# Performance work log

Measured on AMD Instinct MI355X. Metric: run time of the kernel, lower is better.

The kernel has to match this reference:

```python
import jax, jax.numpy as jnp
import numpy as np

HEADS = 16
CHUNK = 128  # chunked (mathematically exact) form of the causal cumsum linear attention
EPS = 0.001


def _linear_attention(q, k, v):
    # q, k, v: (B, H, L, d); q, k already SiLU-featurized
    B, H, L, d = q.shape
    Nc = L // CHUNK
    qc = q.reshape(B, H, Nc, CHUNK, d)
    kc = k.reshape(B, H, Nc, CHUNK, d)
    vc = v.reshape(B, H, Nc, CHUNK, d)

    # inter-chunk running state: S = cumsum of k (x) v over previous chunks, z = cumsum of k
    kv_chunk = jnp.einsum('bhncd,bhnce->bhnde', kc, vc)        # (B,H,Nc,d,d)
    S = jnp.cumsum(kv_chunk, axis=2) - kv_chunk                 # exclusive cumsum
    k_sum = kc.sum(axis=3)                                      # (B,H,Nc,d)
    z = jnp.cumsum(k_sum, axis=2) - k_sum                       # exclusive cumsum

    # intra-chunk causal part
    scores = jnp.einsum('bhnid,bhnjd->bhnij', qc, kc)           # (B,H,Nc,C,C)
    mask = jnp.tril(jnp.ones((CHUNK, CHUNK), dtype=bool))
    scores = jnp.where(mask, scores, jnp.zeros((), scores.dtype))
    num = jnp.einsum('bhnij,bhnje->bhnie', scores, vc)
    num = num + jnp.einsum('bhnid,bhnde->bhnie', qc, S)

    k_cum_local = jnp.cumsum(kc, axis=3)                        # within-chunk cumsum of k
    den = jnp.einsum('bhnid,bhnid->bhni', qc, k_cum_local)
    den = den + jnp.einsum('bhnid,bhnd->bhni', qc, z)

    out = num / jnp.maximum(den, EPS)[..., None]
    return out.reshape(B, H, L, d)


def setup_inputs() -> dict:
    key = jax.random.key(0)
    ks = jax.random.split(key, 9)
    D = 1024
    B, L = 4, 2048
    s = 0.02  # init scale
    return {
        'x':  jax.random.normal(ks[0], (B, L, D), dtype=jnp.float32),
        'Wq': jax.random.normal(ks[1], (D, D), dtype=jnp.float32) * s,
        'bq': jnp.zeros((D,), dtype=jnp.float32),
        'Wk': jax.random.normal(ks[2], (D, D), dtype=jnp.float32) * s,
        'bk': jnp.zeros((D,), dtype=jnp.float32),
        'Wv': jax.random.normal(ks[3], (D, D), dtype=jnp.float32) * s,
        'bv': jnp.zeros((D,), dtype=jnp.float32),
        'Wo': jax.random.normal(ks[4], (D, D), dtype=jnp.float32) * s,
        'bo': jnp.zeros((D,), dtype=jnp.float32),
    }


def reference(x, Wq, bq, Wk, bk, Wv, bv, Wo, bo):
    B, L, D = x.shape
    H = HEADS
    d = D // H
    # torch Linear: y = x @ W.T + b
    q = jax.nn.silu(x @ Wq.T + bq).reshape(B, L, H, d).transpose(0, 2, 1, 3)
    k = jax.nn.silu(x @ Wk.T + bk).reshape(B, L, H, d).transpose(0, 2, 1, 3)
    v = (x @ Wv.T + bv).reshape(B, L, H, d).transpose(0, 2, 1, 3)
    out = _linear_attention(q, k, v)                  # (B,H,L,d)
    out = out.transpose(0, 2, 1, 3).reshape(B, L, D)
    return out @ Wo.T + bo
```

## Files before the change

### kernel.cpp

```cpp
#include <hip/hip_runtime.h>
#include <math.h>

#define D_MODEL 1024
#define HEADS   16
#define HDIM    64
#define CHUNK   128
#define B_SZ    4
#define L_SEQ   2048
#define NCHUNK  16
#define NTOK    8192
#define EPS_DEN 1e-3f

typedef _Float16 half8 __attribute__((ext_vector_type(8)));
typedef float    f32x4 __attribute__((ext_vector_type(4)));

__device__ __forceinline__ void gld_lds16(const void* g, void* l) {
    __builtin_amdgcn_global_load_lds(
        (const __attribute__((address_space(1))) void*)g,
        (__attribute__((address_space(3))) void*)l, 16, 0, 0);
}

__global__ __launch_bounds__(256) void prep(
    const float* __restrict__ x,  const float* __restrict__ Wq,
    const float* __restrict__ Wk, const float* __restrict__ Wv,
    const float* __restrict__ Wo, const float* __restrict__ bq,
    const float* __restrict__ bk,
    _Float16* __restrict__ x2,  _Float16* __restrict__ w2q,
    _Float16* __restrict__ w2k, _Float16* __restrict__ wv16,
    _Float16* __restrict__ wo16, float* __restrict__ bqk) {
    const int bid = blockIdx.x;
    if (bid < 5120) {
        const float* src; _Float16* dst; int t;
        if (bid < 4096)      { src = x;  dst = x2;  t = bid * 256 + threadIdx.x; }
        else if (bid < 4608) { src = Wq; dst = w2q; t = (bid - 4096) * 256 + threadIdx.x; }
        else                 { src = Wk; dst = w2k; t = (bid - 4608) * 256 + threadIdx.x; }
        int m = t >> 7, kc = (t & 127) << 3;
        const float* s = src + (size_t)m * 1024 + kc;
        f32x4 a = *(const f32x4*)s;
        f32x4 b = *(const f32x4*)(s + 4);
        float xs[8] = {a.x, a.y, a.z, a.w, b.x, b.y, b.z, b.w};
        half8 hi, lo;
        #pragma unroll
        for (int u = 0; u < 8; ++u) {
            _Float16 h = (_Float16)xs[u];
            hi[u] = h;
            lo[u] = (_Float16)(xs[u] - (float)h);
        }
        *(half8*)(dst + (size_t)m * 2048 + kc)        = hi;
        *(half8*)(dst + (size_t)m * 2048 + 1024 + kc) = lo;
    } else if (bid < 6144) {
        const float* src; _Float16* dst; int t;
        if (bid < 5632) { src = Wv; dst = wv16; t = (bid - 5120) * 256 + threadIdx.x; }
        else            { src = Wo; dst = wo16; t = (bid - 5632) * 256 + threadIdx.x; }
        int m = t >> 7, kc = (t & 127) << 3;
        const float* s = src + (size_t)m * 1024 + kc;
        f32x4 a = *(const f32x4*)s;
        f32x4 b = *(const f32x4*)(s + 4);
        float xs[8] = {a.x, a.y, a.z, a.w, b.x, b.y, b.z, b.w};
        half8 hv;
        #pragma unroll
        for (int u = 0; u < 8; ++u) hv[u] = (_Float16)xs[u];
        *(half8*)(dst + (size_t)m * 1024 + kc) = hv;
    } else {
        int i = (bid - 6144) * 256 + threadIdx.x;
        bqk[i] = (i < 1024) ? bq[i] : bk[i - 1024];
    }
}

__global__ __launch_bounds__(256, 4) void gemm_qk(
    const _Float16* __restrict__ A,
    const _Float16* __restrict__ B,
    const float* __restrict__ bqk,
    float* __restrict__ Q32, float* __restrict__ K32,
    _Float16* __restrict__ Q16, _Float16* __restrict__ K16) {
    __shared__ __align__(16) _Float16 sA[4096];
    __shared__ __align__(16) _Float16 sB[4096];
    __shared__ __align__(16) _Float16 sC16[32 * 136];

    const int tid  = threadIdx.x;
    const int lane = tid & 63;
    const int w    = tid >> 6;
    const int row0 = blockIdx.x * 128;
    const int col0 = blockIdx.y * 128;
    const int wm   = (w & 1) * 64;
    const int wn   = (w >> 1) * 64;

    const int ch0 = w * 64 + lane;
    const int rS0 = ch0 >> 2;
    const int cS0 = (ch0 & 3) ^ ((rS0 >> 1) & 3);
    const int ch1 = ch0 + 256;
    const int rS1 = ch1 >> 2;
    const int cS1 = (ch1 & 3) ^ ((rS1 >> 1) & 3);

    f32x4 acc[4][4];
    #pragma unroll
    for (int i = 0; i < 4; ++i)
        #pragma unroll
        for (int j = 0; j < 4; ++j) { f32x4 z = {0.f, 0.f, 0.f, 0.f}; acc[i][j] = z; }

    const int ml = lane & 15;
    const int kg = lane >> 4;
    int offA[4], offB[4];
    #pragma unroll
    for (int i = 0; i < 4; ++i) {
        int r  = wm + i * 16 + ml;
        offA[i] = r * 32 + (kg ^ ((r >> 1) & 3)) * 8;
        int rn = wn + i * 16 + ml;
        offB[i] = rn * 32 + (kg ^ ((rn >> 1) & 3)) * 8;
    }

    for (int kit = 0; kit < 96; ++kit) {
        const int k0   = kit * 32;
        const int acol = (k0 < 2048) ? k0 : k0 - 2048;
        const int bcol = (k0 < 1024) ? k0 : k0 - 1024;

        gld_lds16(A + (size_t)(row0 + rS0) * 2048 + acol + cS0 * 8, &sA[w * 512]);
        gld_lds16(A + (size_t)(row0 + rS1) * 2048 + acol + cS1 * 8, &sA[2048 + w * 512]);
        gld_lds16(B + (size_t)(col0 + rS0) * 2048 + bcol + cS0 * 8, &sB[w * 512]);
        gld_lds16(B + (size_t)(col0 + rS1) * 2048 + bcol + cS1 * 8, &sB[2048 + w * 512]);
        __syncthreads();

        half8 af[4], bf[4];
        #pragma unroll
        for (int i = 0; i < 4; ++i) {
            af[i] = *(const half8*)&sA[offA[i]];
            bf[i] = *(const half8*)&sB[offB[i]];
        }
        #pragma unroll
        for (int i = 0; i < 4; ++i)
            #pragma unroll
            for (int j = 0; j < 4; ++j)
                acc[i][j] = __builtin_amdgcn_mfma_f32_16x16x32_f16(af[i], bf[j], acc[i][j], 0, 0, 0);
        __syncthreads();
    }

    const int colq = (col0 < 1024) ? col0 : col0 - 1024;
    float*    Y32  = (col0 < 1024) ? Q32 : K32;
    _Float16* Y16  = (col0 < 1024) ? Q16 : K16;

    const int rg = lane >> 4;
    #pragma unroll
    for (int j = 0; j < 4; ++j) {
        const float bv = bqk[col0 + wn + j * 16 + ml];
        const int nn = colq + wn + j * 16 + ml;
        #pragma unroll
        for (int i = 0; i < 4; ++i) {
            #pragma unroll
            for (int t = 0; t < 4; ++t) {
                float vv = acc[i][j][t] + bv;
                vv = vv / (1.f + expf(-vv));
                acc[i][j][t] = vv;
                int mm = row0 + wm + i * 16 + rg * 4 + t;
                Y32[(size_t)mm * 1024 + nn] = vv;
            }
        }
    }
    for (int s = 0; s < 4; ++s) {
        if ((wm == 0) == (s < 2)) {
            const int ib = (s & 1) * 2;
            #pragma unroll
            for (int ii = 0; ii < 2; ++ii)
                #pragma unroll
                for (int j = 0; j < 4; ++j)
                    #pragma unroll
                    for (int t = 0; t < 4; ++t) {
                        int lr = ii * 16 + rg * 4 + t;
                        sC16[lr * 136 + wn + j * 16 + ml] = (_Float16)acc[ib + ii][j][t];
                    }
        }
        __syncthreads();
        #pragma unroll
        for (int u = 0; u < 2; ++u) {
            int c = u * 256 + tid;
            int r = c >> 4, cc = (c & 15) * 8;
            half8 hv = *(const half8*)&sC16[r * 136 + cc];
            *(half8*)(Y16 + (size_t)(row0 + 32 * s + r) * 1024 + colq + cc) = hv;
        }
        __syncthreads();
    }
}

template<int KITERS, int ACT, int W32, int W16>
__global__ __launch_bounds__(256, 4) void gemm_f16(
    const _Float16* __restrict__ A, int lda,
    const _Float16* __restrict__ B, int ldb,
    const float* __restrict__ bias,
    float* __restrict__ Y32, _Float16* __restrict__ Y16, float outscale) {
    __shared__ __align__(16) _Float16 sA[4096];
    __shared__ __align__(16) _Float16 sB[4096];
    __shared__ __align__(16) _Float16 sC16[32 * 136];

    const int tid  = threadIdx.x;
    const int lane = tid & 63;
    const int w    = tid >> 6;
    const int row0 = blockIdx.x * 128;
    const int col0 = blockIdx.y * 128;
    const int wm   = (w & 1) * 64;
    const int wn   = (w >> 1) * 64;

    const int ch0 = w * 64 + lane;
    const int rS0 = ch0 >> 2;
    const int cS0 = (ch0 & 3) ^ ((rS0 >> 1) & 3);
    const int ch1 = ch0 + 256;
    const int rS1 = ch1 >> 2;
    const int cS1 = (ch1 & 3) ^ ((rS1 >> 1) & 3);

    f32x4 acc[4][4];
    #pragma unroll
    for (int i = 0; i < 4; ++i)
        #pragma unroll
        for (int j = 0; j < 4; ++j) { f32x4 z = {0.f, 0.f, 0.f, 0.f}; acc[i][j] = z; }

    const int ml = lane & 15;
    const int kg = lane >> 4;
    int offA[4], offB[4];
    #pragma unroll
    for (int i = 0; i < 4; ++i) {
        int r  = wm + i * 16 + ml;
        offA[i] = r * 32 + (kg ^ ((r >> 1) & 3)) * 8;
        int rn = wn + i * 16 + ml;
        offB[i] = rn * 32 + (kg ^ ((rn >> 1) & 3)) * 8;
    }

    for (int kit = 0; kit < KITERS; ++kit) {
        const int k0 = kit * 32;
        gld_lds16(A + (size_t)(row0 + rS0) * lda + k0 + cS0 * 8, &sA[w * 512]);
        gld_lds16(A + (size_t)(row0 + rS1) * lda + k0 + cS1 * 8, &sA[2048 + w * 512]);
        gld_lds16(B + (size_t)(col0 + rS0) * ldb + k0 + cS0 * 8, &sB[w * 512]);
        gld_lds16(B + (size_t)(col0 + rS1) * ldb + k0 + cS1 * 8, &sB[2048 + w * 512]);
        __syncthreads();

        half8 af[4], bf[4];
        #pragma unroll
        for (int i = 0; i < 4; ++i) {
            af[i] = *(const half8*)&sA[offA[i]];
            bf[i] = *(const half8*)&sB[offB[i]];
        }
        #pragma unroll
        for (int i = 0; i < 4; ++i)
            #pragma unroll
            for (int j = 0; j < 4; ++j)
                acc[i][j] = __builtin_amdgcn_mfma_f32_16x16x32_f16(af[i], bf[j], acc[i][j], 0, 0, 0);
        __syncthreads();
    }

    const int rg = lane >> 4;
    #pragma unroll
    for (int j = 0; j < 4; ++j) {
        const int nn = col0 + wn + j * 16 + ml;
        const float bv = bias[nn];
        #pragma unroll
        for (int i = 0; i < 4; ++i) {
            #pragma unroll
            for (int t = 0; t < 4; ++t) {
                float vv = acc[i][j][t] * outscale + bv;
                if (ACT) vv = vv / (1.f + expf(-vv));
                acc[i][j][t] = vv;
                if (W32) {
                    int mm = row0 + wm + i * 16 + rg * 4 + t;
                    Y32[(size_t)mm * 1024 + nn] = vv;
                }
            }
        }
    }
    if (W16) {
        for (int s = 0; s < 4; ++s) {
            if ((wm == 0) == (s < 2)) {
                const int ib = (s & 1) * 2;
                #pragma unroll
                for (int ii = 0; ii < 2; ++ii)
                    #pragma unroll
                    for (int j = 0; j < 4; ++j)
                        #pragma unroll
                        for (int t = 0; t < 4; ++t) {
                            int lr = ii * 16 + rg * 4 + t;
                            sC16[lr * 136 + wn + j * 16 + ml] = (_Float16)acc[ib + ii][j][t];
                        }
            }
            __syncthreads();
            #pragma unroll
            for (int u = 0; u < 2; ++u) {
                int c = u * 256 + tid;
                int r = c >> 4, cc = (c & 15) * 8;
                half8 hv = *(const half8*)&sC16[r * 136 + cc];
                *(half8*)(Y16 + (size_t)(row0 + 32 * s + r) * 1024 + col0 + cc) = hv;
            }
            __syncthreads();
        }
    }
}

__global__ __launch_bounds__(256) void chunk_stats(
    const _Float16* __restrict__ k16g, const _Float16* __restrict__ v16g,
    const float* __restrict__ kf32,
    float* __restrict__ kvT, float* __restrict__ ksum) {
    const int blk = blockIdx.x;
    const int n = blk & 15, bh = blk >> 4, h = bh & 15, b = bh >> 4;
    const size_t base = ((size_t)b * L_SEQ + (size_t)n * CHUNK) * D_MODEL + (size_t)h * HDIM;

    __shared__ __align__(16) _Float16 sv[64 * 136];
    __shared__ __align__(16) _Float16 sk[64 * 136];
    __shared__ float sred[4 * 64];

    const int tid = threadIdx.x;
    #pragma unroll
    for (int p = 0; p < 4; ++p) {
        int idx = p * 256 + tid;
        int j = idx >> 3, c = idx & 7;
        half8 vv = *(const half8*)(v16g + base + (size_t)j * D_MODEL + c * 8);
        half8 kk = *(const half8*)(k16g + base + (size_t)j * D_MODEL + c * 8);
        #pragma unroll
        for (int u = 0; u < 8; ++u) {
            sv[(c * 8 + u) * 136 + j] = vv[u];
            sk[(c * 8 + u) * 136 + j] = kk[u];
        }
    }
    __syncthreads();

    const int lane = tid & 63;
    const int w    = tid >> 6;
    const int ml   = lane & 15;
    const int kg   = lane >> 4;

    f32x4 acc[4];
    #pragma unroll
    for (int ft = 0; ft < 4; ++ft) { f32x4 z = {0.f,0.f,0.f,0.f}; acc[ft] = z; }
    #pragma unroll
    for (int ft = 0; ft < 4; ++ft)
        #pragma unroll
        for (int kit = 0; kit < 4; ++kit) {
            half8 af = *(const half8*)&sv[(w * 16 + ml) * 136 + kit * 32 + kg * 8];
            half8 bf = *(const half8*)&sk[(ft * 16 + ml) * 136 + kit * 32 + kg * 8];
            acc[ft] = __builtin_amdgcn_mfma_f32_16x16x32_f16(af, bf, acc[ft], 0, 0, 0);
        }
    float* o = kvT + (size_t)blk * 4096;
    #pragma unroll
    for (int ft = 0; ft < 4; ++ft)
        #pragma unroll
        for (int t = 0; t < 4; ++t) {
            int e = w * 16 + kg * 4 + t;
            o[e * 64 + ft * 16 + ml] = acc[ft][t];
        }

    float s = 0.f;
    for (int j = w * 32; j < w * 32 + 32; ++j)
        s += kf32[base + (size_t)j * D_MODEL + lane];
    sred[w * 64 + lane] = s;
    __syncthreads();
    if (tid < 64)
        ksum[(size_t)blk * 64 + tid] = sred[tid] + sred[64 + tid] + sred[128 + tid] + sred[192 + tid];
}

__global__ __launch_bounds__(256) void scan_chunks(float* __restrict__ kvT,
                                                   float* __restrict__ ksum) {
    const int bh  = blockIdx.x >> 4;
    const int seg = blockIdx.x & 15;
    const int idx = seg * 256 + threadIdx.x;
    float* base = kvT + (size_t)bh * NCHUNK * 4096 + idx;
    float run = 0.f;
    #pragma unroll
    for (int nn = 0; nn < NCHUNK; ++nn) {
        float t = base[(size_t)nn * 4096];
        base[(size_t)nn * 4096] = run;
        run += t;
    }
    if (seg == 0 && threadIdx.x < 64) {
        float* zb = ksum + (size_t)bh * NCHUNK * 64 + threadIdx.x;
        float r2 = 0.f;
        #pragma unroll
        for (int nn = 0; nn < NCHUNK; ++nn) {
            float t = zb[nn * 64];
            zb[nn * 64] = r2;
            r2 += t;
        }
    }
}

__global__ __launch_bounds__(256) void den_kernel(
    const float* __restrict__ qf32, const float* __restrict__ kf32,
    const float* __restrict__ zg, float* __restrict__ deng) {
    const int blk = blockIdx.x;
    const int n = blk & 15, bh = blk >> 4, h = bh & 15, b = bh >> 4;
    const size_t base = ((size_t)b * L_SEQ + (size_t)n * CHUNK) * D_MODEL + (size_t)h * HDIM;

    __shared__ float skk[128 * 64];
    __shared__ float part[4 * 64];

    const int tid = threadIdx.x;
    #pragma unroll
    for (int p = 0; p < 8; ++p) {
        int idx = p * 256 + tid;
        int j = idx >> 4, fc = (idx & 15) * 4;
        *(f32x4*)&skk[j * 64 + fc] = *(const f32x4*)(kf32 + base + (size_t)j * D_MODEL + fc);
    }
    __syncthreads();

    const int w = tid >> 6, lane = tid & 63;
    float ps = 0.f;
    for (int j = w * 32; j < w * 32 + 32; ++j) ps += skk[j * 64 + lane];
    part[w * 64 + lane] = ps;
    __syncthreads();

    float acc = zg[(size_t)blk * 64 + lane];
    for (int w2 = 0; w2 < w; ++w2) acc += part[w2 * 64 + lane];

    float* dout = deng + ((size_t)(b * 16 + h)) * L_SEQ + n * CHUNK;
    for (int jj = 0; jj < 32; ++jj) {
        int j = w * 32 + jj;
        acc += skk[j * 64 + lane];
        float d = qf32[base + (size_t)j * D_MODEL + lane] * acc;
        #pragma unroll
        for (int off = 32; off > 0; off >>= 1) d += __shfl_xor(d, off, 64);
        if (lane == 0) dout[j] = d;
    }
}

__global__ __launch_bounds__(256) void attn_core(
    const _Float16* __restrict__ q16g, const _Float16* __restrict__ k16g,
    const _Float16* __restrict__ v16g, const float* __restrict__ STg,
    const float* __restrict__ deng, _Float16* __restrict__ O16) {
    const int blk = blockIdx.x;
    const int n = blk & 15, bh = blk >> 4, h = bh & 15, b = bh >> 4;
    const size_t base = ((size_t)b * L_SEQ + (size_t)n * CHUNK) * D_MODEL + (size_t)h * HDIM;

    __shared__ __align__(16) _Float16 sq [128 * 72];
    __shared__ __align__(16) _Float16 sk [128 * 72];
    __shared__ __align__(16) _Float16 sv [64 * 136];
    __shared__ __align__(16) _Float16 sS [64 * 72];
    __shared__ __align__(16) _Float16 ssc[64 * 136];
    __shared__ float sden[128];

    const int tid = threadIdx.x;
    #pragma unroll
    for (int p = 0; p < 4; ++p) {
        int idx = p * 256 + tid;
        int j = idx >> 3, c = idx & 7;
        *(half8*)&sq[j * 72 + c * 8] = *(const half8*)(q16g + base + (size_t)j * D_MODEL + c * 8);
        *(half8*)&sk[j * 72 + c * 8] = *(const half8*)(k16g + base + (size_t)j * D_MODEL + c * 8);
        half8 vv = *(const half8*)(v16g + base + (size_t)j * D_MODEL + c * 8);
        #pragma unroll
        for (int u = 0; u < 8; ++u) sv[(c * 8 + u) * 136 + j] = vv[u];
    }
    #pragma unroll
    for (int p = 0; p < 2; ++p) {
        int idx = p * 256 + tid;
        int e = idx >> 3, c = idx & 7;
        f32x4 a = *(const f32x4*)(STg + (size_t)blk * 4096 + e * 64 + c * 8);
        f32x4 b4 = *(const f32x4*)(STg + (size_t)blk * 4096 + e * 64 + c * 8 + 4);
        half8 hv;
        hv[0] = (_Float16)a.x;  hv[1] = (_Float16)a.y;
        hv[2] = (_Float16)a.z;  hv[3] = (_Float16)a.w;
        hv[4] = (_Float16)b4.x; hv[5] = (_Float16)b4.y;
        hv[6] = (_Float16)b4.z; hv[7] = (_Float16)b4.w;
        *(half8*)&sS[e * 72 + c * 8] = hv;
    }
    if (tid < 128) sden[tid] = deng[((size_t)(b * 16 + h)) * L_SEQ + n * CHUNK + tid];
    __syncthreads();

    const int lane = tid & 63;
    const int w    = tid >> 6;
    const int ml   = lane & 15;
    const int kg   = lane >> 4;

    for (int h2 = 0; h2 < 2; ++h2) {
        const int r0 = h2 * 64 + w * 16;
        const int rowmax = r0 + 15;

        f32x4 acc1[8];
        #pragma unroll
        for (int nt = 0; nt < 8; ++nt) { f32x4 z = {0.f,0.f,0.f,0.f}; acc1[nt] = z; }
        #pragma unroll
        for (int nt = 0; nt < 8; ++nt) {
            if (nt * 16 <= rowmax) {
                #pragma unroll
                for (int kit = 0; kit < 2; ++kit) {
                    half8 af = *(const half8*)&sq[(r0 + ml) * 72 + kit * 32 + kg * 8];
                    half8 bf = *(const half8*)&sk[(nt * 16 + ml) * 72 + kit * 32 + kg * 8];
                    acc1[nt] = __builtin_amdgcn_mfma_f32_16x16x32_f16(af, bf, acc1[nt], 0, 0, 0);
                }
            }
        }
        #pragma unroll
        for (int nt = 0; nt < 8; ++nt) {
            #pragma unroll
            for (int t = 0; t < 4; ++t) {
                int lr = w * 16 + kg * 4 + t;
                int ig = h2 * 64 + lr;
                int jg = nt * 16 + ml;
                float val = (jg <= ig) ? acc1[nt][t] : 0.f;
                ssc[lr * 136 + jg] = (_Float16)val;
            }
        }
        __syncthreads();

        f32x4 acc2[4];
        #pragma unroll
        for (int et = 0; et < 4; ++et) { f32x4 z = {0.f,0.f,0.f,0.f}; acc2[et] = z; }
        const int nkit = (h2 == 0) ? 2 : 4;
        #pragma unroll
        for (int et = 0; et < 4; ++et) {
            for (int kit = 0; kit < nkit; ++kit) {
                half8 af = *(const half8*)&ssc[(w * 16 + ml) * 136 + kit * 32 + kg * 8];
                half8 bf = *(const half8*)&sv[(et * 16 + ml) * 136 + kit * 32 + kg * 8];
                acc2[et] = __builtin_amdgcn_mfma_f32_16x16x32_f16(af, bf, acc2[et], 0, 0, 0);
            }
            #pragma unroll
            for (int kit = 0; kit < 2; ++kit) {
                half8 af = *(const half8*)&sq[(r0 + ml) * 72 + kit * 32 + kg * 8];
                half8 bf = *(const half8*)&sS[(et * 16 + ml) * 72 + kit * 32 + kg * 8];
                acc2[et] = __builtin_amdgcn_mfma_f32_16x16x32_f16(af, bf, acc2[et], 0, 0, 0);
            }
        }
        #pragma unroll
        for (int t = 0; t < 4; ++t) {
            int lr = w * 16 + kg * 4 + t;
            int ig = h2 * 64 + lr;
            float rc = 0.015625f / fmaxf(sden[ig], EPS_DEN);
            #pragma unroll
            for (int et = 0; et < 4; ++et) {
                int e = et * 16 + ml;
                O16[base + (size_t)ig * D_MODEL + e] = (_Float16)(acc2[et][t] * rc);
            }
        }
        __syncthreads();
    }
}

extern "C" void kernel_launch(void* const* d_in, const int* in_sizes, int n_in,
                              void* d_out, int out_size, void* d_ws, size_t ws_size,
                              hipStream_t stream) {
    const float* x  = (const float*)d_in[0];
    const float* Wq = (const float*)d_in[1];
    const float* bq = (const float*)d_in[2];
    const float* Wk = (const float*)d_in[3];
    const float* bk = (const float*)d_in[4];
    const float* Wv = (const float*)d_in[5];
    const float* bv = (const float*)d_in[6];
    const float* Wo = (const float*)d_in[7];
    const float* bo = (const float*)d_in[8];
    float* out = (float*)d_out;

    char* p = (char*)d_ws;
    _Float16* x2   = (_Float16*)p;  p += (size_t)NTOK * 2048 * 2;
    _Float16* w2q  = (_Float16*)p;  p += (size_t)1024 * 2048 * 2;
    _Float16* w2k  = (_Float16*)p;  p += (size_t)1024 * 2048 * 2;
    _Float16* wv16 = (_Float16*)p;  p += (size_t)1024 * 1024 * 2;
    _Float16* wo16 = (_Float16*)p;  p += (size_t)1024 * 1024 * 2;
    float* qf   = (float*)p;        p += (size_t)NTOK * 1024 * 4;
    float* kf   = (float*)p;        p += (size_t)NTOK * 1024 * 4;
    _Float16* q16 = (_Float16*)p;   p += (size_t)NTOK * 1024 * 2;
    _Float16* k16 = (_Float16*)p;   p += (size_t)NTOK * 1024 * 2;
    _Float16* v16 = (_Float16*)p;   p += (size_t)NTOK * 1024 * 2;
    float* kvT  = (float*)p;        p += (size_t)1024 * 4096 * 4;
    float* ksb  = (float*)p;        p += (size_t)1024 * 64 * 4;
    float* den  = (float*)p;        p += (size_t)B_SZ * HEADS * L_SEQ * 4;
    float* bqk  = (float*)p;        p += 2048 * 4;
    _Float16* attn16 = x2;

    prep<<<6152, 256, 0, stream>>>(x, Wq, Wk, Wv, Wo, bq, bk,
                                   x2, w2q, w2k, wv16, wo16, bqk);

    gemm_qk<<<dim3(64, 16), 256, 0, stream>>>(x2, w2q, bqk, qf, kf, q16, k16);
    gemm_f16<32, 0, 0, 1><<<dim3(64, 8), 256, 0, stream>>>(x2, 2048, wv16, 1024, bv,
                                                           nullptr, v16, 1.f);

    chunk_stats<<<1024, 256, 0, stream>>>(k16, v16, kf, kvT, ksb);
    scan_chunks<<<1024, 256, 0, stream>>>(kvT, ksb);
    den_kernel<<<1024, 256, 0, stream>>>(qf, kf, ksb, den);
    attn_core<<<1024, 256, 0, stream>>>(q16, k16, v16, kvT, den, attn16);

    gemm_f16<32, 0, 1, 0><<<dim3(64, 8), 256, 0, stream>>>(attn16, 1024, wo16, 1024, bo,
                                                           out, nullptr, 64.f);
}
```

Baseline: 354.1 us.

## Merge QK and V projections into one launch; shrink output GEMM tiles

Fuses the V projection GEMM into the QK GEMM kernel as extra column blocks. The grid is reordered so column blocks vary fastest, so blocks sharing the same A rows are scheduled together. The output projection becomes a dedicated kernel with 128x64 tiles, giving 1024 blocks instead of 512 to fill more CUs. The cost removed is one launch plus tail under-occupancy, at the price of uneven block lengths (96 vs 32 k-iterations) in the merged launch and less reuse per output tile.

```diff
diff --git a/kernel.cpp b/kernel.cpp
--- a/kernel.cpp
+++ b/kernel.cpp
@@ -67,23 +67,32 @@
     }
 }
 
-__global__ __launch_bounds__(256, 4) void gemm_qk(
+__global__ __launch_bounds__(256, 4) void gemm_qkv(
     const _Float16* __restrict__ A,
-    const _Float16* __restrict__ B,
-    const float* __restrict__ bqk,
+    const _Float16* __restrict__ Bqk,
+    const _Float16* __restrict__ Bv,
+    const float* __restrict__ bqk, const float* __restrict__ bv,
     float* __restrict__ Q32, float* __restrict__ K32,
-    _Float16* __restrict__ Q16, _Float16* __restrict__ K16) {
+    _Float16* __restrict__ Q16, _Float16* __restrict__ K16,
+    _Float16* __restrict__ V16) {
     __shared__ __align__(16) _Float16 sA[4096];
     __shared__ __align__(16) _Float16 sB[4096];
     __shared__ __align__(16) _Float16 sC16[32 * 136];
 
+    const int cb   = blockIdx.x;
+    const int isqk = (cb < 16);
     const int tid  = threadIdx.x;
     const int lane = tid & 63;
     const int w    = tid >> 6;
-    const int row0 = blockIdx.x * 128;
-    const int col0 = blockIdx.y * 128;
+    const int row0 = blockIdx.y * 128;
+    const int col0 = cb * 128;
     const int wm   = (w & 1) * 64;
     const int wn   = (w >> 1) * 64;
+
+    const _Float16* B = isqk ? Bqk : Bv;
+    const int ldb     = isqk ? 2048 : 1024;
+    const int bcol0   = isqk ? col0 : col0 - 2048;
+    const int kits    = isqk ? 96 : 32;
 
     const int ch0 = w * 64 + lane;
     const int rS0 = ch0 >> 2;
@@ -109,15 +118,15 @@
         offB[i] = rn * 32 + (kg ^ ((rn >> 1) & 3)) * 8;
     }
 
-    for (int kit = 0; kit < 96; ++kit) {
+    for (int kit = 0; kit < kits; ++kit) {
         const int k0   = kit * 32;
         const int acol = (k0 < 2048) ? k0 : k0 - 2048;
         const int bcol = (k0 < 1024) ? k0 : k0 - 1024;
 
         gld_lds16(A + (size_t)(row0 + rS0) * 2048 + acol + cS0 * 8, &sA[w * 512]);
         gld_lds16(A + (size_t)(row0 + rS1) * 2048 + acol + cS1 * 8, &sA[2048 + w * 512]);
-        gld_lds16(B + (size_t)(col0 + rS0) * 2048 + bcol + cS0 * 8, &sB[w * 512]);
-        gld_lds16(B + (size_t)(col0 + rS1) * 2048 + bcol + cS1 * 8, &sB[2048 + w * 512]);
+        gld_lds16(B + (size_t)(bcol0 + rS0) * ldb + bcol + cS0 * 8, &sB[w * 512]);
+        gld_lds16(B + (size_t)(bcol0 + rS1) * ldb + bcol + cS1 * 8, &sB[2048 + w * 512]);
         __syncthreads();
 
         half8 af[4], bf[4];
@@ -134,24 +143,27 @@
         __syncthreads();
     }
 
-    const int colq = (col0 < 1024) ? col0 : col0 - 1024;
+    const int colq = isqk ? ((col0 < 1024) ? col0 : col0 - 1024) : (col0 - 2048);
     float*    Y32  = (col0 < 1024) ? Q32 : K32;
-    _Float16* Y16  = (col0 < 1024) ? Q16 : K16;
+    _Float16* Y16  = isqk ? ((col0 < 1024) ? Q16 : K16) : V16;
 
     const int rg = lane >> 4;
     #pragma unroll
     for (int j = 0; j < 4; ++j) {
-        const float bv = bqk[col0 + wn + j * 16 + ml];
+        const float bvb = isqk ? bqk[col0 + wn + j * 16 + ml]
+                               : bv[colq + wn + j * 16 + ml];
         const int nn = colq + wn + j * 16 + ml;
         #pragma unroll
         for (int i = 0; i < 4; ++i) {
             #pragma unroll
             for (int t = 0; t < 4; ++t) {
-                float vv = acc[i][j][t] + bv;
-                vv = vv / (1.f + expf(-vv));
+                float vv = acc[i][j][t] + bvb;
+                if (isqk) {
+                    vv = vv / (1.f + expf(-vv));
+                    int mm = row0 + wm + i * 16 + rg * 4 + t;
+                    Y32[(size_t)mm * 1024 + nn] = vv;
+                }
                 acc[i][j][t] = vv;
-                int mm = row0 + wm + i * 16 + rg * 4 + t;
-                Y32[(size_t)mm * 1024 + nn] = vv;
             }
         }
     }
@@ -180,23 +192,19 @@
     }
 }
 
-template<int KITERS, int ACT, int W32, int W16>
-__global__ __launch_bounds__(256, 4) void gemm_f16(
-    const _Float16* __restrict__ A, int lda,
-    const _Float16* __restrict__ B, int ldb,
+__global__ __launch_bounds__(256, 4) void gemm_out(
+    const _Float16* __restrict__ A,
+    const _Float16* __restrict__ B,
     const float* __restrict__ bias,
-    float* __restrict__ Y32, _Float16* __restrict__ Y16, float outscale) {
+    float* __restrict__ Y) {
     __shared__ __align__(16) _Float16 sA[4096];
-    __shared__ __align__(16) _Float16 sB[4096];
-    __shared__ __align__(16) _Float16 sC16[32 * 136];
+    __shared__ __align__(16) _Float16 sB[2048];
 
     const int tid  = threadIdx.x;
     const int lane = tid & 63;
     const int w    = tid >> 6;
-    const int row0 = blockIdx.x * 128;
-    const int col0 = blockIdx.y * 128;
-    const int wm   = (w & 1) * 64;
-    const int wn   = (w >> 1) * 64;
+    const int col0 = blockIdx.x * 64;
+    const int row0 = blockIdx.y * 128;
 
     const int ch0 = w * 64 + lane;
     const int rS0 = ch0 >> 2;
@@ -205,39 +213,40 @@
     const int rS1 = ch1 >> 2;
     const int cS1 = (ch1 & 3) ^ ((rS1 >> 1) & 3);
 
-    f32x4 acc[4][4];
-    #pragma unroll
-    for (int i = 0; i < 4; ++i)
+    f32x4 acc[2][4];
+    #pragma unroll
+    for (int i = 0; i < 2; ++i)
         #pragma unroll
         for (int j = 0; j < 4; ++j) { f32x4 z = {0.f, 0.f, 0.f, 0.f}; acc[i][j] = z; }
 
     const int ml = lane & 15;
     const int kg = lane >> 4;
-    int offA[4], offB[4];
-    #pragma unroll
-    for (int i = 0; i < 4; ++i) {
-        int r  = wm + i * 16 + ml;
+    int offA[2], offB[4];
+    #pragma unroll
+    for (int i = 0; i < 2; ++i) {
+        int r  = w * 32 + i * 16 + ml;
         offA[i] = r * 32 + (kg ^ ((r >> 1) & 3)) * 8;
-        int rn = wn + i * 16 + ml;
-        offB[i] = rn * 32 + (kg ^ ((rn >> 1) & 3)) * 8;
-    }
-
-    for (int kit = 0; kit < KITERS; ++kit) {
+    }
+    #pragma unroll
+    for (int j = 0; j < 4; ++j) {
+        int rn = j * 16 + ml;
+        offB[j] = rn * 32 + (kg ^ ((rn >> 1) & 3)) * 8;
+    }
+
+    for (int kit = 0; kit < 32; ++kit) {
         const int k0 = kit * 32;
-        gld_lds16(A + (size_t)(row0 + rS0) * lda + k0 + cS0 * 8, &sA[w * 512]);
-        gld_lds16(A + (size_t)(row0 + rS1) * lda + k0 + cS1 * 8, &sA[2048 + w * 512]);
-        gld_lds16(B + (size_t)(col0 + rS0) * ldb + k0 + cS0 * 8, &sB[w * 512]);
-        gld_lds16(B + (size_t)(col0 + rS1) * ldb + k0 + cS1 * 8, &sB[2048 + w * 512]);
-        __syncthreads();
-
-        half8 af[4], bf[4];
-        #pragma unroll
-        for (int i = 0; i < 4; ++i) {
-            af[i] = *(const half8*)&sA[offA[i]];
-            bf[i] = *(const half8*)&sB[offB[i]];
-        }
-        #pragma unroll
-        for (int i = 0; i < 4; ++i)
+        gld_lds16(A + (size_t)(row0 + rS0) * 1024 + k0 + cS0 * 8, &sA[w * 512]);
+        gld_lds16(A + (size_t)(row0 + rS1) * 1024 + k0 + cS1 * 8, &sA[2048 + w * 512]);
+        gld_lds16(B + (size_t)(col0 + rS0) * 1024 + k0 + cS0 * 8, &sB[w * 512]);
+        __syncthreads();
+
+        half8 af[2], bf[4];
+        #pragma unroll
+        for (int i = 0; i < 2; ++i) af[i] = *(const half8*)&sA[offA[i]];
+        #pragma unroll
+        for (int j = 0; j < 4; ++j) bf[j] = *(const half8*)&sB[offB[j]];
+        #pragma unroll
+        for (int i = 0; i < 2; ++i)
             #pragma unroll
             for (int j = 0; j < 4; ++j)
                 acc[i][j] = __builtin_amdgcn_mfma_f32_16x16x32_f16(af[i], bf[j], acc[i][j], 0, 0, 0);
@@ -247,45 +256,15 @@
     const int rg = lane >> 4;
     #pragma unroll
     for (int j = 0; j < 4; ++j) {
-        const int nn = col0 + wn + j * 16 + ml;
-        const float bv = bias[nn];
-        #pragma unroll
-        for (int i = 0; i < 4; ++i) {
+        const int nn = col0 + j * 16 + ml;
+        const float bvb = bias[nn];
+        #pragma unroll
+        for (int i = 0; i < 2; ++i) {
             #pragma unroll
             for (int t = 0; t < 4; ++t) {
-                float vv = acc[i][j][t] * outscale + bv;
-                if (ACT) vv = vv / (1.f + expf(-vv));
-                acc[i][j][t] = vv;
-                if (W32) {
-                    int mm = row0 + wm + i * 16 + rg * 4 + t;
-                    Y32[(size_t)mm * 1024 + nn] = vv;
-                }
-            }
-        }
-    }
-    if (W16) {
-        for (int s = 0; s < 4; ++s) {
-            if ((wm == 0) == (s < 2)) {
-                const int ib = (s & 1) * 2;
-                #pragma unroll
-                for (int ii = 0; ii < 2; ++ii)
-                    #pragma unroll
-                    for (int j = 0; j < 4; ++j)
-                        #pragma unroll
-                        for (int t = 0; t < 4; ++t) {
-                            int lr = ii * 16 + rg * 4 + t;
-                            sC16[lr * 136 + wn + j * 16 + ml] = (_Float16)acc[ib + ii][j][t];
-                        }
-            }
-            __syncthreads();
-            #pragma unroll
-            for (int u = 0; u < 2; ++u) {
-                int c = u * 256 + tid;
-                int r = c >> 4, cc = (c & 15) * 8;
-                half8 hv = *(const half8*)&sC16[r * 136 + cc];
-                *(half8*)(Y16 + (size_t)(row0 + 32 * s + r) * 1024 + col0 + cc) = hv;
-            }
-            __syncthreads();
+                int mm = row0 + w * 32 + i * 16 + rg * 4 + t;
+                Y[(size_t)mm * 1024 + nn] = acc[i][j][t] * 64.f + bvb;
+            }
         }
     }
 }
@@ -560,15 +539,13 @@
     prep<<<6152, 256, 0, stream>>>(x, Wq, Wk, Wv, Wo, bq, bk,
                                    x2, w2q, w2k, wv16, wo16, bqk);
 
-    gemm_qk<<<dim3(64, 16), 256, 0, stream>>>(x2, w2q, bqk, qf, kf, q16, k16);
-    gemm_f16<32, 0, 0, 1><<<dim3(64, 8), 256, 0, stream>>>(x2, 2048, wv16, 1024, bv,
-                                                           nullptr, v16, 1.f);
+    gemm_qkv<<<dim3(24, 64), 256, 0, stream>>>(x2, w2q, wv16, bqk, bv,
+                                               qf, kf, q16, k16, v16);
 
     chunk_stats<<<1024, 256, 0, stream>>>(k16, v16, kf, kvT, ksb);
     scan_chunks<<<1024, 256, 0, stream>>>(kvT, ksb);
     den_kernel<<<1024, 256, 0, stream>>>(qf, kf, ksb, den);
     attn_core<<<1024, 256, 0, stream>>>(q16, k16, v16, kvT, den, attn16);
 
-    gemm_f16<32, 0, 1, 0><<<dim3(64, 8), 256, 0, stream>>>(attn16, 1024, wo16, 1024, bo,
-                                                           out, nullptr, 64.f);
-}
+    gemm_out<<<dim3(16, 64), 256, 0, stream>>>(attn16, wo16, bo, out);
+}
```

After: 388.8 us. 9.8% more time.
